# Optimization experiments

Hardware: AMD Instinct MI355X
Metric: run time of the kernel (lower is better)

Reference implementation:

```python
import jax, jax.numpy as jnp
import numpy as np

B, T, N, SD, D, HYP, EMB = 128, 256, 8, 200, 64, 64, 32

def _ln(x, g, b, eps=1e-5):
    mu = jnp.mean(x, -1, keepdims=True)
    v = jnp.mean((x - mu) ** 2, -1, keepdims=True)
    return (x - mu) * jax.lax.rsqrt(v + eps) * g + b

def setup_inputs():
    key = jax.random.key(0)
    ks = iter(jax.random.split(key, 64))
    def p(shape, scale=0.05):
        return (jax.random.normal(next(ks), shape) * scale).astype(jnp.float32)
    n, sd, d, hyp, emb = N, SD, D, HYP, EMB
    return dict(
        qvals=p((B, T, n), 1.0), states=p((B, T, sd), 1.0), hidden_state=p((B, T, n, d), 1.0),
        enc_w1=p((sd, d)), enc_b1=p((d,)), enc_w2=p((d, d)), enc_b2=p((d,)),
        wq=p((d, d)), bq=p((d,)), wk=p((d, d)), bk=p((d,)), wv=p((d, d)), bv=p((d,)),
        wo=p((d, d)), bo=p((d,)),
        ln1_g=jnp.ones((d,), jnp.float32), ln1_b=jnp.zeros((d,), jnp.float32),
        ffn_w1=p((d, d)), ffn_b1=p((d,)), ffn_w2=p((d, d)), ffn_b2=p((d,)),
        ln2_g=jnp.ones((d,), jnp.float32), ln2_b=jnp.zeros((d,), jnp.float32),
        fc2ni_w=p((n, d, n - 1)), fc2ni_b=p((n, n - 1)),
        norm_g=jnp.ones((n - 1,), jnp.float32), norm_b=jnp.zeros((n - 1,), jnp.float32),
        w1a=p((2 * d, hyp)), b1a=p((hyp,)), w1b=p((hyp, n * emb)), b1b=p((n * emb,)),
        hb1w=p((2 * d, emb)), hb1b=p((emb,)),
        w2a=p((2 * d, hyp)), b2a=p((hyp,)), w2b=p((hyp, emb)), b2b=p((emb,)),
        hb2w1=p((2 * d, emb)), hb2b1=p((emb,)), hb2w2=p((emb, 1)), hb2b2=p((1,)))

def reference(qvals, states, hidden_state, enc_w1, enc_b1, enc_w2, enc_b2,
              wq, bq, wk, bk, wv, bv, wo, bo, ln1_g, ln1_b,
              ffn_w1, ffn_b1, ffn_w2, ffn_b2, ln2_g, ln2_b,
              fc2ni_w, fc2ni_b, norm_g, norm_b,
              w1a, b1a, w1b, b1b, hb1w, hb1b,
              w2a, b2a, w2b, b2b, hb2w1, hb2b1, hb2w2, hb2b2):
    sg = jax.lax.stop_gradient
    b, t, n = qvals.shape
    bt = b * t
    d = hidden_state.shape[-1]
    emb = hb1w.shape[1]
    # Encoder_s: relu(fc1) then tanh(fc2(e)+e)
    s = states.reshape(bt, -1)
    e = jax.nn.relu(s @ enc_w1 + enc_b1)
    enc = jnp.tanh(e @ enc_w2 + enc_b2 + e)                       # (bt, 64)
    # concat detached agent hiddens with detached state embedding -> (bt, n+1, 64)
    h = jnp.concatenate([sg(hidden_state.reshape(bt, n, d)), sg(enc)[:, None, :]], axis=1)
    # transformer block (single-head self-attention + FFN, post-LN)
    q = h @ wq + bq; k = h @ wk + bk; v = h @ wv + bv
    att = jax.nn.softmax(jnp.einsum('bid,bjd->bij', q, k) / jnp.sqrt(jnp.float32(d)), axis=-1)
    h2 = _ln(h + (att @ v) @ wo + bo, ln1_g, ln1_b)
    h3 = _ln(h2 + jax.nn.relu(h2 @ ffn_w1 + ffn_b1) @ ffn_w2 + ffn_b2, ln2_g, ln2_b)
    h_trans = h3[:, :n]                                           # (bt, n, 64)
    ens = jnp.concatenate([enc, sg(h_trans).mean(1)], axis=-1)    # (bt, 128)
    # per-agent fc2_Ni -> LayerNorm -> sigmoid, vectorized over agents
    ni = jnp.einsum('xnd,nde->xne', h_trans, fc2ni_w) + fc2ni_b   # (bt, n, n-1)
    ni = jax.nn.sigmoid(_ln(ni, norm_g, norm_b))
    # insert 1.0 at the diagonal (agent i keeps its own q with weight 1)
    rows = jnp.arange(n)[:, None]; cols = jnp.arange(n)[None, :]
    gidx = jnp.clip(cols - (cols > rows).astype(jnp.int32), 0, n - 2)  # (n, n)
    gathered = jnp.take_along_axis(ni, jnp.broadcast_to(gidx, (bt, n, n)), axis=-1)
    nfull = jnp.where(cols == rows, jnp.float32(1.0), gathered)   # (bt, n, n)
    N_nn = nfull.reshape(b, t, n, n)
    q_ni = (qvals[:, :, None, :] * N_nn).sum(-1).reshape(bt, 1, n)
    # hypernetwork mixing (QMIX)
    ens_d = sg(ens)
    w1 = jnp.abs(jax.nn.relu(ens_d @ w1a + b1a) @ w1b + b1b).reshape(bt, n, emb)
    b1 = (ens_d @ hb1w + hb1b).reshape(bt, 1, emb)
    w2 = jnp.abs(jax.nn.relu(ens @ w2a + b2a) @ w2b + b2b).reshape(bt, emb, 1)
    b2 = (jax.nn.relu(ens @ hb2w1 + hb2b1) @ hb2w2 + hb2b2).reshape(bt, 1, 1)
    hidden = jax.nn.elu(q_ni @ w1 + b1)
    y = (hidden @ w2 + b2).reshape(b, t, 1)
    eye_mask = jnp.broadcast_to(jnp.eye(n, dtype=bool), (b, t, n, n))
    return y, N_nn, eye_mask
```

## Files before the change

kernel.cpp:

```cpp
#include <hip/hip_runtime.h>
#include <hip/hip_bf16.h>

typedef __bf16 bf16x8 __attribute__((ext_vector_type(8)));
typedef __bf16 bf16x4 __attribute__((ext_vector_type(4)));
typedef float f32x4 __attribute__((ext_vector_type(4)));

#define ROWSG 32768
#define RB 8
#define HPAD 72
#define NN_OFF ((size_t)ROWSG)
#define EYE_OFF ((size_t)ROWSG + (size_t)ROWSG*64)

#define OFF_EW1   0
#define OFF_EW2   14336
#define OFF_WQ    18432
#define OFF_WK    22528
#define OFF_WV    26624
#define OFF_WO    30720
#define OFF_F1    34816
#define OFF_F2    38912
#define OFF_W1A   43008
#define OFF_W1B   51200
#define OFF_HB1W  67584
#define OFF_W2A   71680
#define OFF_W2B   79872
#define OFF_HB2W1 81920
#define WS_TOTAL  86016

__device__ __align__(16) __bf16 g_ws[WS_TOTAL];

#define MFMA16(a,b,c) __builtin_amdgcn_mfma_f32_16x16x32_bf16(a,b,c,0,0,0)

struct TP { const float* src[14]; };

__global__ __launch_bounds__(256) void wtrans(TP tp) {
    const int gid = blockIdx.x * 256 + threadIdx.x;
    if (gid >= WS_TOTAL) return;
    const int OFFS[14] = {OFF_EW1, OFF_EW2, OFF_WQ, OFF_WK, OFF_WV, OFF_WO, OFF_F1,
                          OFF_F2, OFF_W1A, OFF_W1B, OFF_HB1W, OFF_W2A, OFF_W2B, OFF_HB2W1};
    const int KPS[14]  = {224, 64, 64, 64, 64, 64, 64, 64, 128, 64, 128, 128, 64, 128};
    const int KRS[14]  = {200, 64, 64, 64, 64, 64, 64, 64, 128, 64, 128, 128, 64, 128};
    const int NS[14]   = {64, 64, 64, 64, 64, 64, 64, 64, 64, 256, 32, 64, 32, 32};
    int m = 0;
#pragma unroll
    for (int i = 1; i < 14; ++i) if (gid >= OFFS[i]) m = i;
    const int loc = gid - OFFS[m];
    const int Kp = KPS[m];
    const int n = loc / Kp;
    const int k = loc - n * Kp;
    float v = 0.f;
    if (k < KRS[m]) v = tp.src[m][(size_t)k * NS[m] + n];
    g_ws[gid] = (__bf16)v;
}

struct MainP {
    const float *qvals, *states, *hid, *eb1, *eb2, *bq, *bk, *bv, *bo,
        *l1g, *l1b, *fb1, *fb2, *l2g, *l2b, *niw, *nib, *ng, *nb,
        *b1a, *b1b, *hb1b, *b2a, *b2b, *hb2b1, *hw2, *hb2b2;
    float* out;
};

__device__ __forceinline__ void proj_ln(const __bf16* A, const __bf16* WT,
                                        const float* bias, const float* g, const float* bb,
                                        __bf16* H, int w, int quad, int l15) {
    for (int mti = 0; mti < 2; ++mti) {
        const int mt = w + 4 * mti;
        if (mt >= 5) continue;
        f32x4 acc0 = {0,0,0,0}, acc1 = {0,0,0,0}, acc2 = {0,0,0,0}, acc3 = {0,0,0,0};
#pragma unroll
        for (int ks = 0; ks < 2; ++ks) {
            const int kk = ks * 32 + quad * 8;
            const bf16x8 af = *(const bf16x8*)(A + (mt * 16 + l15) * HPAD + kk);
            acc0 = MFMA16(af, *(const bf16x8*)(WT + (size_t)(0 * 16 + l15) * 64 + kk), acc0);
            acc1 = MFMA16(af, *(const bf16x8*)(WT + (size_t)(1 * 16 + l15) * 64 + kk), acc1);
            acc2 = MFMA16(af, *(const bf16x8*)(WT + (size_t)(2 * 16 + l15) * 64 + kk), acc2);
            acc3 = MFMA16(af, *(const bf16x8*)(WT + (size_t)(3 * 16 + l15) * 64 + kk), acc3);
        }
        float v[4][4], g4[4], b4[4];
#pragma unroll
        for (int nt = 0; nt < 4; ++nt) {
            const int col = nt * 16 + l15;
            const float bo = bias[col];
            g4[nt] = g[col]; b4[nt] = bb[col];
            const f32x4 a = (nt == 0) ? acc0 : (nt == 1) ? acc1 : (nt == 2) ? acc2 : acc3;
#pragma unroll
            for (int r = 0; r < 4; ++r)
                v[nt][r] = a[r] + bo + (float)H[(mt * 16 + quad * 4 + r) * HPAD + col];
        }
#pragma unroll
        for (int r = 0; r < 4; ++r) {
            float s  = v[0][r] + v[1][r] + v[2][r] + v[3][r];
            float s2 = v[0][r]*v[0][r] + v[1][r]*v[1][r] + v[2][r]*v[2][r] + v[3][r]*v[3][r];
#pragma unroll
            for (int off = 1; off < 16; off <<= 1) {
                s  += __shfl_xor(s,  off, 64);
                s2 += __shfl_xor(s2, off, 64);
            }
            const float mu  = s * 0.015625f;
            const float var = s2 * 0.015625f - mu * mu;
            const float rs  = rsqrtf(var + 1e-5f);
#pragma unroll
            for (int nt = 0; nt < 4; ++nt)
                H[(mt * 16 + quad * 4 + r) * HPAD + nt * 16 + l15] =
                    (__bf16)((v[nt][r] - mu) * rs * g4[nt] + b4[nt]);
        }
    }
}

__global__ __launch_bounds__(256) void mixer_main(MainP p) {
    __shared__ __bf16 Qb[80 * HPAD];
    __shared__ __bf16 Kb[80 * HPAD];
    __shared__ __bf16 Vb[80 * HPAD];
    __shared__ __bf16 Hb[80 * HPAD];
    __shared__ __bf16 EbU[16 * HPAD];
    __shared__ __bf16 Tb2[16 * HPAD];
    __shared__ __bf16 ensB[16 * 136];
    __shared__ float  attU[8 * 81];
    __shared__ float  sQv[64];
    __shared__ float  qniL[64];
    __shared__ __bf16 W1bS[8 * 256];
    __shared__ float  B1f[8 * 32], W2f[8 * 32], T3f[8 * 32];

    const int blk = blockIdx.x;
    const int bt0 = blk * RB;
    const int t = threadIdx.x;
    const int w = t >> 6, lane = t & 63, quad = lane >> 4, l15 = lane & 15;
    const __bf16* ws = g_ws;

#pragma unroll
    for (int it = 0; it < 4; ++it) {
        const int u = it * 256 + t;
        const int x = u >> 7, rem = u & 127, n = rem >> 4, d4 = (rem & 15) * 4;
        const float4 v4 = *(const float4*)(p.hid + ((size_t)(bt0 + x) * 512 + n * 64 + d4));
        bf16x4 o; o[0] = (__bf16)v4.x; o[1] = (__bf16)v4.y; o[2] = (__bf16)v4.z; o[3] = (__bf16)v4.w;
        *(bf16x4*)(Hb + (x * 9 + n) * HPAD + d4) = o;
    }
    if (t < 64) sQv[t] = p.qvals[(size_t)(bt0 + (t >> 3)) * 8 + (t & 7)];
    __syncthreads();

    float e4[4];
    {
        const int n0 = w * 16;
        int srow = bt0 + l15; if (srow >= ROWSG) srow = ROWSG - 1;
        const float* sp0 = p.states + (size_t)srow * 200;
        f32x4 acc = {0, 0, 0, 0};
        for (int ks = 0; ks < 7; ++ks) {
            const int kk = ks * 32 + quad * 8;
            bf16x8 af;
            if (kk < 200) {
#pragma unroll
                for (int j = 0; j < 8; ++j) af[j] = (__bf16)sp0[kk + j];
            } else {
#pragma unroll
                for (int j = 0; j < 8; ++j) af[j] = (__bf16)0.0f;
            }
            const bf16x8 bf = *(const bf16x8*)(ws + OFF_EW1 + (size_t)(n0 + l15) * 224 + kk);
            acc = MFMA16(af, bf, acc);
        }
        const float b1 = p.eb1[n0 + l15];
#pragma unroll
        for (int r = 0; r < 4; ++r) {
            const float ev = fmaxf(acc[r] + b1, 0.f);
            e4[r] = ev;
            EbU[(quad * 4 + r) * HPAD + n0 + l15] = (__bf16)ev;
        }
    }
    __syncthreads();

    {
        const int n0 = w * 16;
        f32x4 acc = {0, 0, 0, 0};
#pragma unroll
        for (int ks = 0; ks < 2; ++ks) {
            const int kk = ks * 32 + quad * 8;
            const bf16x8 af = *(const bf16x8*)(EbU + l15 * HPAD + kk);
            const bf16x8 bf = *(const bf16x8*)(ws + OFF_EW2 + (size_t)(n0 + l15) * 64 + kk);
            acc = MFMA16(af, bf, acc);
        }
        const float b2 = p.eb2[n0 + l15];
#pragma unroll
        for (int r = 0; r < 4; ++r) {
            const int xr = quad * 4 + r;
            if (xr < RB) {
                const float ev = tanhf(acc[r] + e4[r] + b2);
                Hb[(xr * 9 + 8) * HPAD + n0 + l15] = (__bf16)ev;
                ensB[xr * 136 + n0 + l15] = (__bf16)ev;
            }
        }
    }
    __syncthreads();

    for (int it = 0; it < 15; ++it) {
        const int j = w + 4 * it;
        const int mat = j / 20, r20 = j % 20, mt = r20 >> 2, nt = r20 & 3;
        const __bf16* wt = ws + (mat == 0 ? OFF_WQ : mat == 1 ? OFF_WK : OFF_WV);
        const float* bias = (mat == 0 ? p.bq : mat == 1 ? p.bk : p.bv);
        __bf16* dst = (mat == 0 ? Qb : mat == 1 ? Kb : Vb);
        f32x4 acc = {0, 0, 0, 0};
#pragma unroll
        for (int ks = 0; ks < 2; ++ks) {
            const int kk = ks * 32 + quad * 8;
            const bf16x8 af = *(const bf16x8*)(Hb + (mt * 16 + l15) * HPAD + kk);
            const bf16x8 bf = *(const bf16x8*)(wt + (size_t)(nt * 16 + l15) * 64 + kk);
            acc = MFMA16(af, bf, acc);
        }
        const float bv = bias[nt * 16 + l15];
#pragma unroll
        for (int r = 0; r < 4; ++r)
            dst[(mt * 16 + quad * 4 + r) * HPAD + nt * 16 + l15] = (__bf16)(acc[r] + bv);
    }
    __syncthreads();

    for (int xi = 0; xi < 2; ++xi) {
        const int x = w * 2 + xi;
        for (int base = 0; base < 81; base += 64) {
            const int pidx = base + lane;
            if (pidx < 81) {
                const int i = pidx / 9, jj = pidx - (pidx / 9) * 9;
                const __bf16* qr = Qb + (x * 9 + i) * HPAD;
                const __bf16* kr = Kb + (x * 9 + jj) * HPAD;
                float s = 0.f;
#pragma unroll
                for (int d = 0; d < 64; d += 2) {
                    const unsigned qu = *(const unsigned*)(qr + d);
                    const unsigned ku = *(const unsigned*)(kr + d);
                    const float qlo = __uint_as_float(qu << 16);
                    const float qhi = __uint_as_float(qu & 0xffff0000u);
                    const float klo = __uint_as_float(ku << 16);
                    const float khi = __uint_as_float(ku & 0xffff0000u);
                    s += qlo * klo + qhi * khi;
                }
                attU[x * 81 + pidx] = s * 0.125f;
            }
        }
    }
    __syncthreads();
    if (t < 72) {
        const int x = t / 9, i = t - (t / 9) * 9;
        float* ar = attU + x * 81 + i * 9;
        float m = ar[0];
#pragma unroll
        for (int j = 1; j < 9; ++j) m = fmaxf(m, ar[j]);
        float ssum = 0.f;
#pragma unroll
        for (int j = 0; j < 9; ++j) { const float ex = __expf(ar[j] - m); ar[j] = ex; ssum += ex; }
        const float inv = 1.f / ssum;
#pragma unroll
        for (int j = 0; j < 9; ++j) ar[j] *= inv;
    }
    __syncthreads();

    for (int xi = 0; xi < 2; ++xi) {
        const int x = w * 2 + xi;
        float vreg[9];
#pragma unroll
        for (int jj = 0; jj < 9; ++jj) vreg[jj] = (float)Vb[(x * 9 + jj) * HPAD + lane];
#pragma unroll
        for (int i = 0; i < 9; ++i) {
            float a = 0.f;
#pragma unroll
            for (int jj = 0; jj < 9; ++jj) a += attU[x * 81 + i * 9 + jj] * vreg[jj];
            Qb[(x * 9 + i) * HPAD + lane] = (__bf16)a;
        }
    }
    __syncthreads();

    proj_ln(Qb, ws + OFF_WO, p.bo, p.l1g, p.l1b, Hb, w, quad, l15);
    __syncthreads();

    for (int it = 0; it < 5; ++it) {
        const int j = w + 4 * it;
        const int mt = j >> 2, nt = j & 3;
        f32x4 acc = {0, 0, 0, 0};
#pragma unroll
        for (int ks = 0; ks < 2; ++ks) {
            const int kk = ks * 32 + quad * 8;
            const bf16x8 af = *(const bf16x8*)(Hb + (mt * 16 + l15) * HPAD + kk);
            const bf16x8 bf = *(const bf16x8*)(ws + OFF_F1 + (size_t)(nt * 16 + l15) * 64 + kk);
            acc = MFMA16(af, bf, acc);
        }
        const float fb = p.fb1[nt * 16 + l15];
#pragma unroll
        for (int r = 0; r < 4; ++r)
            Kb[(mt * 16 + quad * 4 + r) * HPAD + nt * 16 + l15] = (__bf16)fmaxf(acc[r] + fb, 0.f);
    }
    __syncthreads();

    proj_ln(Kb, ws + OFF_F2, p.fb2, p.l2g, p.l2b, Hb, w, quad, l15);
    __syncthreads();

#pragma unroll
    for (int it = 0; it < 2; ++it) {
        const int id = it * 256 + t;
        const int x = id >> 6, col = id & 63;
        float s = 0.f;
#pragma unroll
        for (int i = 0; i < 8; ++i) s += (float)Hb[(x * 9 + i) * HPAD + col];
        ensB[x * 136 + 64 + col] = (__bf16)(s * 0.125f);
    }
    __syncthreads();

    {
        const int pr = t >> 2, q4 = t & 3;
        const int x = pr >> 3, n = pr & 7;
        float acc[7] = {0.f, 0.f, 0.f, 0.f, 0.f, 0.f, 0.f};
        const float* wni = p.niw + n * 448;
        for (int dd = 0; dd < 16; ++dd) {
            const int d = q4 * 16 + dd;
            const float hv = (float)Hb[(x * 9 + n) * HPAD + d];
#pragma unroll
            for (int e = 0; e < 7; ++e) acc[e] += hv * wni[d * 7 + e];
        }
#pragma unroll
        for (int e = 0; e < 7; ++e) {
            acc[e] += __shfl_xor(acc[e], 1, 64);
            acc[e] += __shfl_xor(acc[e], 2, 64);
        }
        if (q4 == 0) {
            float s = 0.f;
#pragma unroll
            for (int e = 0; e < 7; ++e) { acc[e] += p.nib[n * 7 + e]; s += acc[e]; }
            const float mu = s * (1.f / 7.f);
            float s2 = 0.f;
#pragma unroll
            for (int e = 0; e < 7; ++e) { const float d0 = acc[e] - mu; s2 += d0 * d0; }
            const float rs = rsqrtf(s2 * (1.f / 7.f) + 1e-5f);
            float* sNi = (float*)EbU;
#pragma unroll
            for (int e = 0; e < 7; ++e) {
                const float vv = (acc[e] - mu) * rs * p.ng[e] + p.nb[e];
                sNi[x * 64 + n * 8 + e] = 1.f / (1.f + __expf(-vv));
            }
        }
    }
    __syncthreads();

    {
        const float* sNi = (const float*)EbU;
        float* Nf = attU;
#pragma unroll
        for (int it = 0; it < 2; ++it) {
            const int id = it * 256 + t;
            const int x = id >> 6, rem = id & 63, i = rem >> 3, jj = rem & 7;
            const float nf = (i == jj) ? 1.f : sNi[x * 64 + i * 8 + (jj - (jj > i ? 1 : 0))];
            p.out[NN_OFF + (size_t)(bt0 + x) * 64 + rem] = nf;
            p.out[EYE_OFF + (size_t)(bt0 + x) * 64 + rem] = (i == jj) ? 1.f : 0.f;
            Nf[x * 64 + rem] = nf;
        }
    }
    __syncthreads();
    {
        const float* Nf = attU;
        const int pr = t >> 2, q4 = t & 3;
        const int x = pr >> 3, i = pr & 7;
        const int j0 = q4 * 2;
        float s = sQv[x * 8 + j0] * Nf[x * 64 + i * 8 + j0] +
                  sQv[x * 8 + j0 + 1] * Nf[x * 64 + i * 8 + j0 + 1];
        s += __shfl_xor(s, 1, 64);
        s += __shfl_xor(s, 2, 64);
        if (q4 == 0) qniL[x * 8 + i] = s;
    }
    __syncthreads();

    {
        const int n0 = w * 16;
#pragma unroll
        for (int m2 = 0; m2 < 2; ++m2) {
            const __bf16* wt = ws + (m2 == 0 ? OFF_W1A : OFF_W2A);
            const float* bias = m2 == 0 ? p.b1a : p.b2a;
            __bf16* dst = m2 == 0 ? EbU : Tb2;
            f32x4 acc = {0, 0, 0, 0};
#pragma unroll
            for (int ks = 0; ks < 4; ++ks) {
                const int kk = ks * 32 + quad * 8;
                const bf16x8 af = *(const bf16x8*)(ensB + l15 * 136 + kk);
                const bf16x8 bf = *(const bf16x8*)(wt + (size_t)(n0 + l15) * 128 + kk);
                acc = MFMA16(af, bf, acc);
            }
            const float bb = bias[n0 + l15];
#pragma unroll
            for (int r = 0; r < 4; ++r)
                dst[(quad * 4 + r) * HPAD + n0 + l15] = (__bf16)fmaxf(acc[r] + bb, 0.f);
        }
    }
    __syncthreads();

    for (int it = 0; it < 6; ++it) {
        const int j = w + 4 * it;
        if (j >= 22) continue;
        int mode, n0, Kp, ksteps, aStride;
        const __bf16 *A, *WT; const float* bias;
        if (j < 16)      { mode = 0; n0 = j * 16;        A = EbU;  aStride = HPAD; WT = ws + OFF_W1B;   bias = p.b1b;  Kp = 64;  ksteps = 2; }
        else if (j < 18) { mode = 1; n0 = (j - 16) * 16; A = ensB; aStride = 136;  WT = ws + OFF_HB1W;  bias = p.hb1b; Kp = 128; ksteps = 4; }
        else if (j < 20) { mode = 2; n0 = (j - 18) * 16; A = Tb2;  aStride = HPAD; WT = ws + OFF_W2B;   bias = p.b2b;  Kp = 64;  ksteps = 2; }
        else             { mode = 3; n0 = (j - 20) * 16; A = ensB; aStride = 136;  WT = ws + OFF_HB2W1; bias = p.hb2b1;Kp = 128; ksteps = 4; }
        f32x4 acc = {0, 0, 0, 0};
        for (int ks = 0; ks < ksteps; ++ks) {
            const int kk = ks * 32 + quad * 8;
            const bf16x8 af = *(const bf16x8*)(A + l15 * aStride + kk);
            const bf16x8 bf = *(const bf16x8*)(WT + (size_t)(n0 + l15) * Kp + kk);
            acc = MFMA16(af, bf, acc);
        }
        const float bb = bias[n0 + l15];
#pragma unroll
        for (int r = 0; r < 4; ++r) {
            const int xr = quad * 4 + r;
            if (xr < RB) {
                const float val = acc[r] + bb;
                if (mode == 0)      W1bS[xr * 256 + n0 + l15] = (__bf16)fabsf(val);
                else if (mode == 1) B1f[xr * 32 + n0 + l15] = val;
                else if (mode == 2) W2f[xr * 32 + n0 + l15] = fabsf(val);
                else                T3f[xr * 32 + n0 + l15] = fmaxf(val, 0.f);
            }
        }
    }
    __syncthreads();

    if (t < 128) {
        const int x = t >> 4, sub = t & 15;
        float pp = 0.f, pb = 0.f;
#pragma unroll
        for (int h2i = 0; h2i < 2; ++h2i) {
            const int e = sub + h2i * 16;
            float a = B1f[x * 32 + e];
#pragma unroll
            for (int i = 0; i < 8; ++i) a += qniL[x * 8 + i] * (float)W1bS[x * 256 + i * 32 + e];
            const float hid = a > 0.f ? a : (__expf(a) - 1.f);
            pp += hid * W2f[x * 32 + e];
            pb += T3f[x * 32 + e] * p.hw2[e];
        }
#pragma unroll
        for (int off = 1; off < 16; off <<= 1) {
            pp += __shfl_xor(pp, off, 64);
            pb += __shfl_xor(pb, off, 64);
        }
        if (sub == 0) p.out[bt0 + x] = pp + pb + p.hb2b2[0];
    }
}

extern "C" void kernel_launch(void* const* d_in, const int* in_sizes, int n_in,
                              void* d_out, int out_size, void* d_ws, size_t ws_size,
                              hipStream_t stream) {
    TP tp;
    tp.src[0]  = (const float*)d_in[3];
    tp.src[1]  = (const float*)d_in[5];
    tp.src[2]  = (const float*)d_in[7];
    tp.src[3]  = (const float*)d_in[9];
    tp.src[4]  = (const float*)d_in[11];
    tp.src[5]  = (const float*)d_in[13];
    tp.src[6]  = (const float*)d_in[17];
    tp.src[7]  = (const float*)d_in[19];
    tp.src[8]  = (const float*)d_in[27];
    tp.src[9]  = (const float*)d_in[29];
    tp.src[10] = (const float*)d_in[31];
    tp.src[11] = (const float*)d_in[33];
    tp.src[12] = (const float*)d_in[35];
    tp.src[13] = (const float*)d_in[37];
    wtrans<<<(WS_TOTAL + 255) / 256, 256, 0, stream>>>(tp);

    MainP p;
    p.qvals = (const float*)d_in[0];
    p.states = (const float*)d_in[1];
    p.hid = (const float*)d_in[2];
    p.eb1 = (const float*)d_in[4];
    p.eb2 = (const float*)d_in[6];
    p.bq = (const float*)d_in[8];
    p.bk = (const float*)d_in[10];
    p.bv = (const float*)d_in[12];
    p.bo = (const float*)d_in[14];
    p.l1g = (const float*)d_in[15];
    p.l1b = (const float*)d_in[16];
    p.fb1 = (const float*)d_in[18];
    p.fb2 = (const float*)d_in[20];
    p.l2g = (const float*)d_in[21];
    p.l2b = (const float*)d_in[22];
    p.niw = (const float*)d_in[23];
    p.nib = (const float*)d_in[24];
    p.ng = (const float*)d_in[25];
    p.nb = (const float*)d_in[26];
    p.b1a = (const float*)d_in[28];
    p.b1b = (const float*)d_in[30];
    p.hb1b = (const float*)d_in[32];
    p.b2a = (const float*)d_in[34];
    p.b2b = (const float*)d_in[36];
    p.hb2b1 = (const float*)d_in[38];
    p.hw2 = (const float*)d_in[39];
    p.hb2b2 = (const float*)d_in[40];
    p.out = (float*)d_out;

    mixer_main<<<ROWSG / RB, 256, 0, stream>>>(p);
}
```

Measured before the change: 439.4 us.

## Reassociate V projection after attention, use MFMA for scores, stage states in LDS

The value projection now runs after attention as (A·H)·Wv + bv instead of A·(H·Wv + bv). This is exact because the softmax rows sum to one, and it removes the Vb buffer and one projection pass before attention. The per-lane scalar QK dot products and the separate softmax pass are replaced by one 16x16 MFMA per row group, with the softmax done through in-register shuffle reductions, which removes a barrier. State rows are loaded with coalesced float4 reads into LDS (reusing W1bS) instead of per-lane scalar global loads inside the encoder MFMA loop. The risk is a small change in bf16 rounding order from the reassociation.

```diff
diff --git a/kernel.cpp b/kernel.cpp
--- a/kernel.cpp
+++ b/kernel.cpp
@@ -108,17 +108,16 @@
 }
 
 __global__ __launch_bounds__(256) void mixer_main(MainP p) {
-    __shared__ __bf16 Qb[80 * HPAD];
-    __shared__ __bf16 Kb[80 * HPAD];
-    __shared__ __bf16 Vb[80 * HPAD];
-    __shared__ __bf16 Hb[80 * HPAD];
-    __shared__ __bf16 EbU[16 * HPAD];
-    __shared__ __bf16 Tb2[16 * HPAD];
-    __shared__ __bf16 ensB[16 * 136];
+    __shared__ __align__(16) __bf16 Hb[80 * HPAD];
+    __shared__ __align__(16) __bf16 Qb[80 * HPAD];
+    __shared__ __align__(16) __bf16 Kb[80 * HPAD];
+    __shared__ __align__(16) __bf16 EbU[16 * HPAD];
+    __shared__ __align__(16) __bf16 Tb2[16 * HPAD];
+    __shared__ __align__(16) __bf16 ensB[16 * 136];
     __shared__ float  attU[8 * 81];
     __shared__ float  sQv[64];
     __shared__ float  qniL[64];
-    __shared__ __bf16 W1bS[8 * 256];
+    __shared__ __align__(16) __bf16 W1bS[8 * 256];
     __shared__ float  B1f[8 * 32], W2f[8 * 32], T3f[8 * 32];
 
     const int blk = blockIdx.x;
@@ -126,6 +125,7 @@
     const int t = threadIdx.x;
     const int w = t >> 6, lane = t & 63, quad = lane >> 4, l15 = lane & 15;
     const __bf16* ws = g_ws;
+    __bf16* Sb = W1bS;
 
 #pragma unroll
     for (int it = 0; it < 4; ++it) {
@@ -135,25 +135,28 @@
         bf16x4 o; o[0] = (__bf16)v4.x; o[1] = (__bf16)v4.y; o[2] = (__bf16)v4.z; o[3] = (__bf16)v4.w;
         *(bf16x4*)(Hb + (x * 9 + n) * HPAD + d4) = o;
     }
+#pragma unroll
+    for (int it = 0; it < 2; ++it) {
+        const int u = it * 256 + t;
+        if (u < 400) {
+            const int xr = u / 50, c4 = u - xr * 50;
+            const float4 v4 = *(const float4*)(p.states + (size_t)(bt0 + xr) * 200 + c4 * 4);
+            bf16x4 o; o[0] = (__bf16)v4.x; o[1] = (__bf16)v4.y; o[2] = (__bf16)v4.z; o[3] = (__bf16)v4.w;
+            *(bf16x4*)(Sb + xr * 224 + c4 * 4) = o;
+        }
+    }
+    if (t < 192) { const int xr = t / 24, c = t - xr * 24; Sb[xr * 224 + 200 + c] = (__bf16)0.0f; }
     if (t < 64) sQv[t] = p.qvals[(size_t)(bt0 + (t >> 3)) * 8 + (t & 7)];
     __syncthreads();
 
     float e4[4];
     {
         const int n0 = w * 16;
-        int srow = bt0 + l15; if (srow >= ROWSG) srow = ROWSG - 1;
-        const float* sp0 = p.states + (size_t)srow * 200;
+        const int srow = (l15 < 8) ? l15 : 7;
         f32x4 acc = {0, 0, 0, 0};
         for (int ks = 0; ks < 7; ++ks) {
             const int kk = ks * 32 + quad * 8;
-            bf16x8 af;
-            if (kk < 200) {
-#pragma unroll
-                for (int j = 0; j < 8; ++j) af[j] = (__bf16)sp0[kk + j];
-            } else {
-#pragma unroll
-                for (int j = 0; j < 8; ++j) af[j] = (__bf16)0.0f;
-            }
+            const bf16x8 af = *(const bf16x8*)(Sb + srow * 224 + kk);
             const bf16x8 bf = *(const bf16x8*)(ws + OFF_EW1 + (size_t)(n0 + l15) * 224 + kk);
             acc = MFMA16(af, bf, acc);
         }
@@ -190,12 +193,12 @@
     }
     __syncthreads();
 
-    for (int it = 0; it < 15; ++it) {
+    for (int it = 0; it < 10; ++it) {
         const int j = w + 4 * it;
         const int mat = j / 20, r20 = j % 20, mt = r20 >> 2, nt = r20 & 3;
-        const __bf16* wt = ws + (mat == 0 ? OFF_WQ : mat == 1 ? OFF_WK : OFF_WV);
-        const float* bias = (mat == 0 ? p.bq : mat == 1 ? p.bk : p.bv);
-        __bf16* dst = (mat == 0 ? Qb : mat == 1 ? Kb : Vb);
+        const __bf16* wt = ws + (mat == 0 ? OFF_WQ : OFF_WK);
+        const float* bias = (mat == 0 ? p.bq : p.bk);
+        __bf16* dst = (mat == 0 ? Qb : Kb);
         f32x4 acc = {0, 0, 0, 0};
 #pragma unroll
         for (int ks = 0; ks < 2; ++ks) {
@@ -213,40 +216,29 @@
 
     for (int xi = 0; xi < 2; ++xi) {
         const int x = w * 2 + xi;
-        for (int base = 0; base < 81; base += 64) {
-            const int pidx = base + lane;
-            if (pidx < 81) {
-                const int i = pidx / 9, jj = pidx - (pidx / 9) * 9;
-                const __bf16* qr = Qb + (x * 9 + i) * HPAD;
-                const __bf16* kr = Kb + (x * 9 + jj) * HPAD;
-                float s = 0.f;
-#pragma unroll
-                for (int d = 0; d < 64; d += 2) {
-                    const unsigned qu = *(const unsigned*)(qr + d);
-                    const unsigned ku = *(const unsigned*)(kr + d);
-                    const float qlo = __uint_as_float(qu << 16);
-                    const float qhi = __uint_as_float(qu & 0xffff0000u);
-                    const float klo = __uint_as_float(ku << 16);
-                    const float khi = __uint_as_float(ku & 0xffff0000u);
-                    s += qlo * klo + qhi * khi;
-                }
-                attU[x * 81 + pidx] = s * 0.125f;
-            }
-        }
-    }
-    __syncthreads();
-    if (t < 72) {
-        const int x = t / 9, i = t - (t / 9) * 9;
-        float* ar = attU + x * 81 + i * 9;
-        float m = ar[0];
-#pragma unroll
-        for (int j = 1; j < 9; ++j) m = fmaxf(m, ar[j]);
-        float ssum = 0.f;
-#pragma unroll
-        for (int j = 0; j < 9; ++j) { const float ex = __expf(ar[j] - m); ar[j] = ex; ssum += ex; }
-        const float inv = 1.f / ssum;
-#pragma unroll
-        for (int j = 0; j < 9; ++j) ar[j] *= inv;
+        const int arow = (x * 9 + l15) * HPAD;
+        f32x4 acc = {0, 0, 0, 0};
+#pragma unroll
+        for (int ks = 0; ks < 2; ++ks) {
+            const int kk = ks * 32 + quad * 8;
+            const bf16x8 qa = *(const bf16x8*)(Qb + arow + kk);
+            const bf16x8 kb = *(const bf16x8*)(Kb + arow + kk);
+            acc = MFMA16(qa, kb, acc);
+        }
+#pragma unroll
+        for (int r = 0; r < 4; ++r) {
+            const int i = quad * 4 + r;
+            float s = (l15 < 9) ? acc[r] * 0.125f : -3.0e38f;
+            float m = s;
+#pragma unroll
+            for (int off = 1; off < 16; off <<= 1) m = fmaxf(m, __shfl_xor(m, off, 64));
+            float e = (l15 < 9) ? __expf(s - m) : 0.f;
+            float sum = e;
+#pragma unroll
+            for (int off = 1; off < 16; off <<= 1) sum += __shfl_xor(sum, off, 64);
+            const float pv = e / sum;
+            if (i < 9 && l15 < 9) attU[x * 81 + i * 9 + l15] = pv;
+        }
     }
     __syncthreads();
 
@@ -254,14 +246,32 @@
         const int x = w * 2 + xi;
         float vreg[9];
 #pragma unroll
-        for (int jj = 0; jj < 9; ++jj) vreg[jj] = (float)Vb[(x * 9 + jj) * HPAD + lane];
+        for (int jj = 0; jj < 9; ++jj) vreg[jj] = (float)Hb[(x * 9 + jj) * HPAD + lane];
 #pragma unroll
         for (int i = 0; i < 9; ++i) {
             float a = 0.f;
 #pragma unroll
             for (int jj = 0; jj < 9; ++jj) a += attU[x * 81 + i * 9 + jj] * vreg[jj];
-            Qb[(x * 9 + i) * HPAD + lane] = (__bf16)a;
-        }
+            Kb[(x * 9 + i) * HPAD + lane] = (__bf16)a;
+        }
+    }
+    __syncthreads();
+
+    for (int it = 0; it < 5; ++it) {
+        const int j = w + 4 * it;
+        const int mt = j >> 2, nt = j & 3;
+        f32x4 acc = {0, 0, 0, 0};
+#pragma unroll
+        for (int ks = 0; ks < 2; ++ks) {
+            const int kk = ks * 32 + quad * 8;
+            const bf16x8 af = *(const bf16x8*)(Kb + (mt * 16 + l15) * HPAD + kk);
+            const bf16x8 bf = *(const bf16x8*)(ws + OFF_WV + (size_t)(nt * 16 + l15) * 64 + kk);
+            acc = MFMA16(af, bf, acc);
+        }
+        const float bv = p.bv[nt * 16 + l15];
+#pragma unroll
+        for (int r = 0; r < 4; ++r)
+            Qb[(mt * 16 + quad * 4 + r) * HPAD + nt * 16 + l15] = (__bf16)(acc[r] + bv);
     }
     __syncthreads();
 
```

Result: no change. 436.9 us (-0.6%).
